# Kernel optimization log

Hardware: AMD Instinct MI355X
Metric: run time of the kernel (lower is better)

Reference implementation:

```python
import jax, jax.numpy as jnp
import numpy as np


def setup_inputs() -> dict:
    key = jax.random.key(0)
    kq, kk, kv = jax.random.split(key, 3)
    B, H, S, D = 2, 16, 2048, 128
    Q = jax.random.normal(kq, (B, H, S, D), dtype=jnp.float32)
    K = jax.random.normal(kk, (B, H, S, D), dtype=jnp.float32)
    V = jax.random.normal(kv, (B, H, S, D), dtype=jnp.float32)
    return {"Q": Q, "K": K, "V": V}


def reference(Q, K, V):
    # Unscaled, unmasked attention: softmax(Q K^T) V
    score = jnp.einsum('bhqd,bhkd->bhqk', Q, K)  # [B,H,S,S]
    attn = jax.nn.softmax(score, axis=-1)
    context = jnp.einsum('bhqk,bhkd->bhqd', attn, V)  # [B,H,S,D]
    return context
```

## Files before the change

kernel.cpp:

```cpp
#include <hip/hip_runtime.h>
#include <stdint.h>

#define BH_N 32
#define S_N  2048
#define D_N  128
#define BK   64
#define NT   (S_N / BK)
#define QW   32
#define BQ   128

#define LOG2E 1.4426950408889634f

typedef __bf16    bf16x8 __attribute__((ext_vector_type(8)));
typedef _Float16  f16x8  __attribute__((ext_vector_type(8)));
typedef float     f32x4  __attribute__((ext_vector_type(4)));

union FragU { uint4 u4; uint32_t u[4]; bf16x8 b; };
union FragH { uint4 u4; uint32_t u[4]; f16x8 h; _Float16 e[8]; };

__device__ __forceinline__ uint32_t pack_bf16(float lo, float hi) {
  uint32_t ul = __float_as_uint(lo) + 0x8000u;
  uint32_t uh = __float_as_uint(hi) + 0x8000u;
  return __builtin_amdgcn_perm(uh, ul, 0x07060302u);
}

__device__ __forceinline__ void gl_lds16(const uint16_t* g, uint16_t* l) {
  __builtin_amdgcn_global_load_lds(
      (const __attribute__((address_space(1))) uint32_t*)g,
      (__attribute__((address_space(3))) uint32_t*)l, 16, 0, 0);
}

__global__ __launch_bounds__(256) void prep_kernel(const float* __restrict__ Kg,
                                                   uint16_t* __restrict__ Ko,
                                                   const float* __restrict__ Vg,
                                                   uint16_t* __restrict__ Vtg) {
  if (blockIdx.x < 4096) {
    const int idx = blockIdx.x * 256 + threadIdx.x;
    const int rg = idx >> 4;
    const int g = idx & 15;
    const float* src = Kg + (size_t)idx * 8;
    float4 a = *(const float4*)(src);
    float4 b = *(const float4*)(src + 4);
    FragH w;
    w.e[0] = (_Float16)a.x; w.e[1] = (_Float16)a.y;
    w.e[2] = (_Float16)a.z; w.e[3] = (_Float16)a.w;
    w.e[4] = (_Float16)b.x; w.e[5] = (_Float16)b.y;
    w.e[6] = (_Float16)b.z; w.e[7] = (_Float16)b.w;
    *(uint4*)(Ko + (size_t)rg * 128 + ((g ^ (rg & 7)) * 8)) = w.u4;
    return;
  }
  __shared__ float stg[64][65];
  const int bid = blockIdx.x - 4096;
  const int dt = bid & 1;
  const int st = (bid >> 1) & 31;
  const int bh = bid >> 6;
  const int tid = threadIdx.x;
  {
    const int r = tid >> 4;
    const int c = (tid & 15) * 4;
    const float* Vb = Vg + ((size_t)bh * S_N + (size_t)st * 64) * D_N + dt * 64;
#pragma unroll
    for (int i = 0; i < 4; ++i) {
      float4 x = *(const float4*)(Vb + (size_t)(r + i * 16) * D_N + c);
      stg[r + i * 16][c + 0] = x.x;
      stg[r + i * 16][c + 1] = x.y;
      stg[r + i * 16][c + 2] = x.z;
      stg[r + i * 16][c + 3] = x.w;
    }
  }
  __syncthreads();
  uint16_t* Vo = Vtg + ((size_t)(bh * 32 + st) * 128 + dt * 64) * 64;
  const int gp = tid & 7;
  const int k0 = (gp & 4) * 8 + (gp & 3) * 4;
#pragma unroll
  for (int it = 0; it < 2; ++it) {
    const int drl = it * 32 + (tid >> 3);
    const int d = dt * 64 + drl;
    uint4 w;
    w.x = pack_bf16(stg[k0 + 0][drl], stg[k0 + 1][drl]);
    w.y = pack_bf16(stg[k0 + 2][drl], stg[k0 + 3][drl]);
    w.z = pack_bf16(stg[k0 + 16][drl], stg[k0 + 17][drl]);
    w.w = pack_bf16(stg[k0 + 18][drl], stg[k0 + 19][drl]);
    *(uint4*)(Vo + (size_t)drl * 64 + ((gp ^ (d & 7)) * 8)) = w;
  }
}

__global__ __launch_bounds__(256, 2)
void attn_kernel(const float* __restrict__ Qg, const uint16_t* __restrict__ Kimg,
                 const uint16_t* __restrict__ Vimg, float* __restrict__ Og) {
  __shared__ uint16_t k_lds[2][BK * 128];
  __shared__ uint16_t vt_lds[2][D_N * 64];

  const int tid = threadIdx.x;
  const int bid = blockIdx.x;
  const int bh = bid & 31;
  const int qb = bid >> 5;
  const int wave = tid >> 6;
  const int lane = tid & 63;
  const int l15 = lane & 15;
  const int quad = lane >> 4;
  const int sw = l15 & 7;

  const float*    Qb = Qg + (size_t)bh * S_N * D_N;
  float*          Ob = Og + (size_t)bh * S_N * D_N;
  const uint16_t* Kt0 = Kimg + (size_t)bh * 32 * 64 * 128;
  const uint16_t* Vt0 = Vimg + (size_t)bh * 32 * 128 * 64;

  const int q0 = qb * BQ + wave * QW;
  const int phase = ((qb << 1) | (bh & 1)) & 31;

  FragH qh[2][4];
#pragma unroll
  for (int g = 0; g < 2; ++g) {
    const float* qrow = Qb + (size_t)(q0 + g * 16 + l15) * D_N + quad * 8;
#pragma unroll
    for (int kc = 0; kc < 4; ++kc) {
      float4 x0 = *(const float4*)(qrow + kc * 32);
      float4 x1 = *(const float4*)(qrow + kc * 32 + 4);
      qh[g][kc].e[0] = (_Float16)(x0.x * LOG2E);
      qh[g][kc].e[1] = (_Float16)(x0.y * LOG2E);
      qh[g][kc].e[2] = (_Float16)(x0.z * LOG2E);
      qh[g][kc].e[3] = (_Float16)(x0.w * LOG2E);
      qh[g][kc].e[4] = (_Float16)(x1.x * LOG2E);
      qh[g][kc].e[5] = (_Float16)(x1.y * LOG2E);
      qh[g][kc].e[6] = (_Float16)(x1.z * LOG2E);
      qh[g][kc].e[7] = (_Float16)(x1.w * LOG2E);
    }
  }

  f32x4 oacc[2][8];
  const f32x4 zf = {0.f, 0.f, 0.f, 0.f};
#pragma unroll
  for (int g = 0; g < 2; ++g)
#pragma unroll
    for (int mt = 0; mt < 8; ++mt) oacc[g][mt] = zf;
  float lsum[2] = {0.f, 0.f};

  const int lel = lane * 8;
  auto stage = [&](int ktp, int buf) {
    const uint16_t* ks = Kt0 + (size_t)ktp * (64 * 128);
    const uint16_t* vs = Vt0 + (size_t)ktp * (128 * 64);
    uint16_t* kl = &k_lds[buf][0];
    uint16_t* vl = &vt_lds[buf][0];
#pragma unroll
    for (int i = 0; i < 4; ++i) {
      const int off = (wave * 16 + i * 4) * 128;
      gl_lds16(ks + off + lel, kl + off + lel);
    }
#pragma unroll
    for (int i = 0; i < 4; ++i) {
      const int off = (wave * 32 + i * 8) * 64;
      gl_lds16(vs + off + lel, vl + off + lel);
    }
  };

  stage(phase, 0);
  asm volatile("s_waitcnt vmcnt(0)" ::: "memory");
  __syncthreads();

#pragma unroll 2
  for (int kt = 0; kt < NT; ++kt) {
    const int cur = kt & 1;
    if (kt + 1 < NT) stage((kt + 1 + phase) & 31, cur ^ 1);

    const uint16_t* kl = &k_lds[cur][0];
    const uint16_t* vl = &vt_lds[cur][0];

    f32x4 sacc[2][4];
    __builtin_amdgcn_s_setprio(1);
#pragma unroll
    for (int kc = 0; kc < 4; ++kc) {
#pragma unroll
      for (int mt = 0; mt < 4; ++mt) {
        FragH a;
        a.u4 = *(const uint4*)(kl + (mt * 16 + l15) * 128 + (((kc * 4 + quad) ^ sw) * 8));
#pragma unroll
        for (int g = 0; g < 2; ++g) {
          f32x4 c = (kc == 0) ? zf : sacc[g][mt];
          sacc[g][mt] = __builtin_amdgcn_mfma_f32_16x16x32_f16(a.h, qh[g][kc].h, c, 0, 0, 0);
        }
      }
    }
    __builtin_amdgcn_s_setprio(0);

#pragma unroll
    for (int half = 0; half < 2; ++half) {
      FragU vf[8];
#pragma unroll
      for (int mt = 0; mt < 8; ++mt)
        vf[mt].u4 = *(const uint4*)(vl + (mt * 16 + l15) * 64 + (((half * 4 + quad) ^ sw) * 8));

      FragU bq[2];
#pragma unroll
      for (int g = 0; g < 2; ++g) {
        const f32x4 s0 = sacc[g][half * 2 + 0];
        const f32x4 s1 = sacc[g][half * 2 + 1];
        float a0 = __builtin_amdgcn_exp2f(s0.x);
        float a1 = __builtin_amdgcn_exp2f(s0.y);
        float a2 = __builtin_amdgcn_exp2f(s0.z);
        float a3 = __builtin_amdgcn_exp2f(s0.w);
        float b0 = __builtin_amdgcn_exp2f(s1.x);
        float b1 = __builtin_amdgcn_exp2f(s1.y);
        float b2 = __builtin_amdgcn_exp2f(s1.z);
        float b3 = __builtin_amdgcn_exp2f(s1.w);
        lsum[g] += ((a0 + a1) + (a2 + a3)) + ((b0 + b1) + (b2 + b3));
        bq[g].u[0] = pack_bf16(a0, a1);
        bq[g].u[1] = pack_bf16(a2, a3);
        bq[g].u[2] = pack_bf16(b0, b1);
        bq[g].u[3] = pack_bf16(b2, b3);
      }
      __builtin_amdgcn_s_setprio(1);
#pragma unroll
      for (int mt = 0; mt < 8; ++mt) {
#pragma unroll
        for (int g = 0; g < 2; ++g) {
          oacc[g][mt] = __builtin_amdgcn_mfma_f32_16x16x32_bf16(vf[mt].b, bq[g].b, oacc[g][mt], 0, 0, 0);
        }
      }
      __builtin_amdgcn_s_setprio(0);
    }

    asm volatile("s_waitcnt vmcnt(0)" ::: "memory");
    __syncthreads();
  }

#pragma unroll
  for (int g = 0; g < 2; ++g) {
    float l = lsum[g];
    l += __shfl_xor(l, 16);
    l += __shfl_xor(l, 32);
    const float rl = 1.0f / l;
#pragma unroll
    for (int mt = 0; mt < 8; ++mt) {
      float4 w;
      w.x = oacc[g][mt].x * rl;
      w.y = oacc[g][mt].y * rl;
      w.z = oacc[g][mt].z * rl;
      w.w = oacc[g][mt].w * rl;
      *(float4*)(Ob + (size_t)(q0 + g * 16 + l15) * D_N + mt * 16 + quad * 4) = w;
    }
  }
}

extern "C" void kernel_launch(void* const* d_in, const int* in_sizes, int n_in,
                              void* d_out, int out_size, void* d_ws, size_t ws_size,
                              hipStream_t stream) {
  const float* Q = (const float*)d_in[0];
  const float* K = (const float*)d_in[1];
  const float* V = (const float*)d_in[2];
  float* O = (float*)d_out;

  const size_t half = (size_t)BH_N * S_N * D_N * sizeof(uint16_t);
  if (ws_size < 2 * half) return;
  uint16_t* Vt = (uint16_t*)d_ws;
  uint16_t* Kh = (uint16_t*)((char*)d_ws + half);

  prep_kernel<<<dim3(4096 + BH_N * 32 * 2), dim3(256), 0, stream>>>(K, Kh, V, Vt);
  attn_kernel<<<dim3(S_N / BQ * BH_N), dim3(256), 0, stream>>>(Q, Kh, Vt, O);
}
```

Before: 195.6 us.

## Software-pipeline QK^T of next tile with softmax and PV of current tile

```diff
diff --git a/kernel.cpp b/kernel.cpp
--- a/kernel.cpp
+++ b/kernel.cpp
@@ -136,17 +136,22 @@
     for (int mt = 0; mt < 8; ++mt) oacc[g][mt] = zf;
   float lsum[2] = {0.f, 0.f};
 
+  f32x4 saccA[2][4];
+  f32x4 saccB[2][4];
+
   const int lel = lane * 8;
-  auto stage = [&](int ktp, int buf) {
+  auto stageK = [&](int ktp, int buf) {
     const uint16_t* ks = Kt0 + (size_t)ktp * (64 * 128);
-    const uint16_t* vs = Vt0 + (size_t)ktp * (128 * 64);
     uint16_t* kl = &k_lds[buf][0];
-    uint16_t* vl = &vt_lds[buf][0];
 #pragma unroll
     for (int i = 0; i < 4; ++i) {
       const int off = (wave * 16 + i * 4) * 128;
       gl_lds16(ks + off + lel, kl + off + lel);
     }
+  };
+  auto stageV = [&](int ktp, int buf) {
+    const uint16_t* vs = Vt0 + (size_t)ktp * (128 * 64);
+    uint16_t* vl = &vt_lds[buf][0];
 #pragma unroll
     for (int i = 0; i < 4; ++i) {
       const int off = (wave * 32 + i * 8) * 64;
@@ -154,19 +159,7 @@
     }
   };
 
-  stage(phase, 0);
-  asm volatile("s_waitcnt vmcnt(0)" ::: "memory");
-  __syncthreads();
-
-#pragma unroll 2
-  for (int kt = 0; kt < NT; ++kt) {
-    const int cur = kt & 1;
-    if (kt + 1 < NT) stage((kt + 1 + phase) & 31, cur ^ 1);
-
-    const uint16_t* kl = &k_lds[cur][0];
-    const uint16_t* vl = &vt_lds[cur][0];
-
-    f32x4 sacc[2][4];
+  auto qk = [&](const uint16_t* kl, f32x4 (&sout_)[2][4]) {
     __builtin_amdgcn_s_setprio(1);
 #pragma unroll
     for (int kc = 0; kc < 4; ++kc) {
@@ -176,25 +169,25 @@
         a.u4 = *(const uint4*)(kl + (mt * 16 + l15) * 128 + (((kc * 4 + quad) ^ sw) * 8));
 #pragma unroll
         for (int g = 0; g < 2; ++g) {
-          f32x4 c = (kc == 0) ? zf : sacc[g][mt];
-          sacc[g][mt] = __builtin_amdgcn_mfma_f32_16x16x32_f16(a.h, qh[g][kc].h, c, 0, 0, 0);
+          f32x4 c = (kc == 0) ? zf : sout_[g][mt];
+          sout_[g][mt] = __builtin_amdgcn_mfma_f32_16x16x32_f16(a.h, qh[g][kc].h, c, 0, 0, 0);
         }
       }
     }
     __builtin_amdgcn_s_setprio(0);
-
+  };
+
+  auto body = [&](int t, f32x4 (&sin_)[2][4], f32x4 (&sout_)[2][4]) {
+    if (t + 2 < NT) stageK((t + 2 + phase) & 31, t & 1);
+    if (t + 1 < NT) stageV((t + 1 + phase) & 31, (t + 1) & 1);
+
+    FragU bq[2][2];
 #pragma unroll
     for (int half = 0; half < 2; ++half) {
-      FragU vf[8];
-#pragma unroll
-      for (int mt = 0; mt < 8; ++mt)
-        vf[mt].u4 = *(const uint4*)(vl + (mt * 16 + l15) * 64 + (((half * 4 + quad) ^ sw) * 8));
-
-      FragU bq[2];
 #pragma unroll
       for (int g = 0; g < 2; ++g) {
-        const f32x4 s0 = sacc[g][half * 2 + 0];
-        const f32x4 s1 = sacc[g][half * 2 + 1];
+        const f32x4 s0 = sin_[g][half * 2 + 0];
+        const f32x4 s1 = sin_[g][half * 2 + 1];
         float a0 = __builtin_amdgcn_exp2f(s0.x);
         float a1 = __builtin_amdgcn_exp2f(s0.y);
         float a2 = __builtin_amdgcn_exp2f(s0.z);
@@ -204,17 +197,28 @@
         float b2 = __builtin_amdgcn_exp2f(s1.z);
         float b3 = __builtin_amdgcn_exp2f(s1.w);
         lsum[g] += ((a0 + a1) + (a2 + a3)) + ((b0 + b1) + (b2 + b3));
-        bq[g].u[0] = pack_bf16(a0, a1);
-        bq[g].u[1] = pack_bf16(a2, a3);
-        bq[g].u[2] = pack_bf16(b0, b1);
-        bq[g].u[3] = pack_bf16(b2, b3);
+        bq[half][g].u[0] = pack_bf16(a0, a1);
+        bq[half][g].u[1] = pack_bf16(a2, a3);
+        bq[half][g].u[2] = pack_bf16(b0, b1);
+        bq[half][g].u[3] = pack_bf16(b2, b3);
       }
+    }
+
+    if (t + 1 < NT) qk(&k_lds[(t + 1) & 1][0], sout_);
+
+    const uint16_t* vl = &vt_lds[t & 1][0];
+#pragma unroll
+    for (int half = 0; half < 2; ++half) {
+      FragU vf[8];
+#pragma unroll
+      for (int mt = 0; mt < 8; ++mt)
+        vf[mt].u4 = *(const uint4*)(vl + (mt * 16 + l15) * 64 + (((half * 4 + quad) ^ sw) * 8));
       __builtin_amdgcn_s_setprio(1);
 #pragma unroll
       for (int mt = 0; mt < 8; ++mt) {
 #pragma unroll
         for (int g = 0; g < 2; ++g) {
-          oacc[g][mt] = __builtin_amdgcn_mfma_f32_16x16x32_bf16(vf[mt].b, bq[g].b, oacc[g][mt], 0, 0, 0);
+          oacc[g][mt] = __builtin_amdgcn_mfma_f32_16x16x32_bf16(vf[mt].b, bq[half][g].b, oacc[g][mt], 0, 0, 0);
         }
       }
       __builtin_amdgcn_s_setprio(0);
@@ -222,6 +226,19 @@
 
     asm volatile("s_waitcnt vmcnt(0)" ::: "memory");
     __syncthreads();
+  };
+
+  stageK(phase, 0);
+  stageV(phase, 0);
+  stageK((1 + phase) & 31, 1);
+  asm volatile("s_waitcnt vmcnt(0)" ::: "memory");
+  __syncthreads();
+  qk(&k_lds[0][0], saccA);
+  __syncthreads();
+
+  for (int t2 = 0; t2 < NT; t2 += 2) {
+    body(t2 + 0, saccA, saccB);
+    body(t2 + 1, saccB, saccA);
   }
 
 #pragma unroll
```

Result: slower. 211.5 us (+8.1%).

## Load V fragments directly from global memory into registers, bypassing LDS

Applied to the files above, without the earlier changes.

```diff
diff --git a/kernel.cpp b/kernel.cpp
--- a/kernel.cpp
+++ b/kernel.cpp
@@ -89,7 +89,6 @@
 void attn_kernel(const float* __restrict__ Qg, const uint16_t* __restrict__ Kimg,
                  const uint16_t* __restrict__ Vimg, float* __restrict__ Og) {
   __shared__ uint16_t k_lds[2][BK * 128];
-  __shared__ uint16_t vt_lds[2][D_N * 64];
 
   const int tid = threadIdx.x;
   const int bid = blockIdx.x;
@@ -137,34 +136,34 @@
   float lsum[2] = {0.f, 0.f};
 
   const int lel = lane * 8;
-  auto stage = [&](int ktp, int buf) {
+  auto stageK = [&](int ktp, int buf) {
     const uint16_t* ks = Kt0 + (size_t)ktp * (64 * 128);
-    const uint16_t* vs = Vt0 + (size_t)ktp * (128 * 64);
     uint16_t* kl = &k_lds[buf][0];
-    uint16_t* vl = &vt_lds[buf][0];
 #pragma unroll
     for (int i = 0; i < 4; ++i) {
       const int off = (wave * 16 + i * 4) * 128;
       gl_lds16(ks + off + lel, kl + off + lel);
     }
-#pragma unroll
-    for (int i = 0; i < 4; ++i) {
-      const int off = (wave * 32 + i * 8) * 64;
-      gl_lds16(vs + off + lel, vl + off + lel);
-    }
   };
 
-  stage(phase, 0);
+  stageK(phase, 0);
   asm volatile("s_waitcnt vmcnt(0)" ::: "memory");
   __syncthreads();
 
 #pragma unroll 2
   for (int kt = 0; kt < NT; ++kt) {
     const int cur = kt & 1;
-    if (kt + 1 < NT) stage((kt + 1 + phase) & 31, cur ^ 1);
+    if (kt + 1 < NT) stageK((kt + 1 + phase) & 31, cur ^ 1);
+
+    const uint16_t* vg = Vt0 + (size_t)((kt + phase) & 31) * (128 * 64);
+    FragU vf0[8], vf1[8];
+#pragma unroll
+    for (int mt = 0; mt < 8; ++mt) {
+      vf0[mt].u4 = *(const uint4*)(vg + (mt * 16 + l15) * 64 + (((0 * 4 + quad) ^ sw) * 8));
+      vf1[mt].u4 = *(const uint4*)(vg + (mt * 16 + l15) * 64 + (((1 * 4 + quad) ^ sw) * 8));
+    }
 
     const uint16_t* kl = &k_lds[cur][0];
-    const uint16_t* vl = &vt_lds[cur][0];
 
     f32x4 sacc[2][4];
     __builtin_amdgcn_s_setprio(1);
@@ -183,18 +182,12 @@
     }
     __builtin_amdgcn_s_setprio(0);
 
-#pragma unroll
-    for (int half = 0; half < 2; ++half) {
-      FragU vf[8];
-#pragma unroll
-      for (int mt = 0; mt < 8; ++mt)
-        vf[mt].u4 = *(const uint4*)(vl + (mt * 16 + l15) * 64 + (((half * 4 + quad) ^ sw) * 8));
-
+    {
       FragU bq[2];
 #pragma unroll
       for (int g = 0; g < 2; ++g) {
-        const f32x4 s0 = sacc[g][half * 2 + 0];
-        const f32x4 s1 = sacc[g][half * 2 + 1];
+        const f32x4 s0 = sacc[g][0];
+        const f32x4 s1 = sacc[g][1];
         float a0 = __builtin_amdgcn_exp2f(s0.x);
         float a1 = __builtin_amdgcn_exp2f(s0.y);
         float a2 = __builtin_amdgcn_exp2f(s0.z);
@@ -214,7 +207,37 @@
       for (int mt = 0; mt < 8; ++mt) {
 #pragma unroll
         for (int g = 0; g < 2; ++g) {
-          oacc[g][mt] = __builtin_amdgcn_mfma_f32_16x16x32_bf16(vf[mt].b, bq[g].b, oacc[g][mt], 0, 0, 0);
+          oacc[g][mt] = __builtin_amdgcn_mfma_f32_16x16x32_bf16(vf0[mt].b, bq[g].b, oacc[g][mt], 0, 0, 0);
+        }
+      }
+      __builtin_amdgcn_s_setprio(0);
+    }
+    {
+      FragU bq[2];
+#pragma unroll
+      for (int g = 0; g < 2; ++g) {
+        const f32x4 s0 = sacc[g][2];
+        const f32x4 s1 = sacc[g][3];
+        float a0 = __builtin_amdgcn_exp2f(s0.x);
+        float a1 = __builtin_amdgcn_exp2f(s0.y);
+        float a2 = __builtin_amdgcn_exp2f(s0.z);
+        float a3 = __builtin_amdgcn_exp2f(s0.w);
+        float b0 = __builtin_amdgcn_exp2f(s1.x);
+        float b1 = __builtin_amdgcn_exp2f(s1.y);
+        float b2 = __builtin_amdgcn_exp2f(s1.z);
+        float b3 = __builtin_amdgcn_exp2f(s1.w);
+        lsum[g] += ((a0 + a1) + (a2 + a3)) + ((b0 + b1) + (b2 + b3));
+        bq[g].u[0] = pack_bf16(a0, a1);
+        bq[g].u[1] = pack_bf16(a2, a3);
+        bq[g].u[2] = pack_bf16(b0, b1);
+        bq[g].u[3] = pack_bf16(b2, b3);
+      }
+      __builtin_amdgcn_s_setprio(1);
+#pragma unroll
+      for (int mt = 0; mt < 8; ++mt) {
+#pragma unroll
+        for (int g = 0; g < 2; ++g) {
+          oacc[g][mt] = __builtin_amdgcn_mfma_f32_16x16x32_bf16(vf1[mt].b, bq[g].b, oacc[g][mt], 0, 0, 0);
         }
       }
       __builtin_amdgcn_s_setprio(0);
```

New measurement: 209.9 us. 1.07x slower.

## Use 8 waves of 16 query rows each instead of 4 waves of 32

Applied to the files above, without the earlier changes.

```diff
diff --git a/kernel.cpp b/kernel.cpp
--- a/kernel.cpp
+++ b/kernel.cpp
@@ -6,7 +6,7 @@
 #define D_N  128
 #define BK   64
 #define NT   (S_N / BK)
-#define QW   32
+#define QW   16
 #define BQ   128
 
 #define LOG2E 1.4426950408889634f
@@ -85,7 +85,7 @@
   }
 }
 
-__global__ __launch_bounds__(256, 2)
+__global__ __launch_bounds__(512, 4)
 void attn_kernel(const float* __restrict__ Qg, const uint16_t* __restrict__ Kimg,
                  const uint16_t* __restrict__ Vimg, float* __restrict__ Og) {
   __shared__ uint16_t k_lds[2][BK * 128];
@@ -109,32 +109,29 @@
   const int q0 = qb * BQ + wave * QW;
   const int phase = ((qb << 1) | (bh & 1)) & 31;
 
-  FragH qh[2][4];
-#pragma unroll
-  for (int g = 0; g < 2; ++g) {
-    const float* qrow = Qb + (size_t)(q0 + g * 16 + l15) * D_N + quad * 8;
+  FragH qh[4];
+  {
+    const float* qrow = Qb + (size_t)(q0 + l15) * D_N + quad * 8;
 #pragma unroll
     for (int kc = 0; kc < 4; ++kc) {
       float4 x0 = *(const float4*)(qrow + kc * 32);
       float4 x1 = *(const float4*)(qrow + kc * 32 + 4);
-      qh[g][kc].e[0] = (_Float16)(x0.x * LOG2E);
-      qh[g][kc].e[1] = (_Float16)(x0.y * LOG2E);
-      qh[g][kc].e[2] = (_Float16)(x0.z * LOG2E);
-      qh[g][kc].e[3] = (_Float16)(x0.w * LOG2E);
-      qh[g][kc].e[4] = (_Float16)(x1.x * LOG2E);
-      qh[g][kc].e[5] = (_Float16)(x1.y * LOG2E);
-      qh[g][kc].e[6] = (_Float16)(x1.z * LOG2E);
-      qh[g][kc].e[7] = (_Float16)(x1.w * LOG2E);
-    }
-  }
-
-  f32x4 oacc[2][8];
+      qh[kc].e[0] = (_Float16)(x0.x * LOG2E);
+      qh[kc].e[1] = (_Float16)(x0.y * LOG2E);
+      qh[kc].e[2] = (_Float16)(x0.z * LOG2E);
+      qh[kc].e[3] = (_Float16)(x0.w * LOG2E);
+      qh[kc].e[4] = (_Float16)(x1.x * LOG2E);
+      qh[kc].e[5] = (_Float16)(x1.y * LOG2E);
+      qh[kc].e[6] = (_Float16)(x1.z * LOG2E);
+      qh[kc].e[7] = (_Float16)(x1.w * LOG2E);
+    }
+  }
+
+  f32x4 oacc[8];
   const f32x4 zf = {0.f, 0.f, 0.f, 0.f};
 #pragma unroll
-  for (int g = 0; g < 2; ++g)
-#pragma unroll
-    for (int mt = 0; mt < 8; ++mt) oacc[g][mt] = zf;
-  float lsum[2] = {0.f, 0.f};
+  for (int mt = 0; mt < 8; ++mt) oacc[mt] = zf;
+  float lsum = 0.f;
 
   const int lel = lane * 8;
   auto stage = [&](int ktp, int buf) {
@@ -143,13 +140,13 @@
     uint16_t* kl = &k_lds[buf][0];
     uint16_t* vl = &vt_lds[buf][0];
 #pragma unroll
-    for (int i = 0; i < 4; ++i) {
-      const int off = (wave * 16 + i * 4) * 128;
+    for (int i = 0; i < 2; ++i) {
+      const int off = (wave * 8 + i * 4) * 128;
       gl_lds16(ks + off + lel, kl + off + lel);
     }
 #pragma unroll
-    for (int i = 0; i < 4; ++i) {
-      const int off = (wave * 32 + i * 8) * 64;
+    for (int i = 0; i < 2; ++i) {
+      const int off = (wave * 16 + i * 8) * 64;
       gl_lds16(vs + off + lel, vl + off + lel);
     }
   };
@@ -166,7 +163,7 @@
     const uint16_t* kl = &k_lds[cur][0];
     const uint16_t* vl = &vt_lds[cur][0];
 
-    f32x4 sacc[2][4];
+    f32x4 sacc[4];
     __builtin_amdgcn_s_setprio(1);
 #pragma unroll
     for (int kc = 0; kc < 4; ++kc) {
@@ -174,11 +171,8 @@
       for (int mt = 0; mt < 4; ++mt) {
         FragH a;
         a.u4 = *(const uint4*)(kl + (mt * 16 + l15) * 128 + (((kc * 4 + quad) ^ sw) * 8));
-#pragma unroll
-        for (int g = 0; g < 2; ++g) {
-          f32x4 c = (kc == 0) ? zf : sacc[g][mt];
-          sacc[g][mt] = __builtin_amdgcn_mfma_f32_16x16x32_f16(a.h, qh[g][kc].h, c, 0, 0, 0);
-        }
+        f32x4 c = (kc == 0) ? zf : sacc[mt];
+        sacc[mt] = __builtin_amdgcn_mfma_f32_16x16x32_f16(a.h, qh[kc].h, c, 0, 0, 0);
       }
     }
     __builtin_amdgcn_s_setprio(0);
@@ -190,11 +184,10 @@
       for (int mt = 0; mt < 8; ++mt)
         vf[mt].u4 = *(const uint4*)(vl + (mt * 16 + l15) * 64 + (((half * 4 + quad) ^ sw) * 8));
 
-      FragU bq[2];
-#pragma unroll
-      for (int g = 0; g < 2; ++g) {
-        const f32x4 s0 = sacc[g][half * 2 + 0];
-        const f32x4 s1 = sacc[g][half * 2 + 1];
+      FragU bq;
+      {
+        const f32x4 s0 = sacc[half * 2 + 0];
+        const f32x4 s1 = sacc[half * 2 + 1];
         float a0 = __builtin_amdgcn_exp2f(s0.x);
         float a1 = __builtin_amdgcn_exp2f(s0.y);
         float a2 = __builtin_amdgcn_exp2f(s0.z);
@@ -203,19 +196,16 @@
         float b1 = __builtin_amdgcn_exp2f(s1.y);
         float b2 = __builtin_amdgcn_exp2f(s1.z);
         float b3 = __builtin_amdgcn_exp2f(s1.w);
-        lsum[g] += ((a0 + a1) + (a2 + a3)) + ((b0 + b1) + (b2 + b3));
-        bq[g].u[0] = pack_bf16(a0, a1);
-        bq[g].u[1] = pack_bf16(a2, a3);
-        bq[g].u[2] = pack_bf16(b0, b1);
-        bq[g].u[3] = pack_bf16(b2, b3);
+        lsum += ((a0 + a1) + (a2 + a3)) + ((b0 + b1) + (b2 + b3));
+        bq.u[0] = pack_bf16(a0, a1);
+        bq.u[1] = pack_bf16(a2, a3);
+        bq.u[2] = pack_bf16(b0, b1);
+        bq.u[3] = pack_bf16(b2, b3);
       }
       __builtin_amdgcn_s_setprio(1);
 #pragma unroll
       for (int mt = 0; mt < 8; ++mt) {
-#pragma unroll
-        for (int g = 0; g < 2; ++g) {
-          oacc[g][mt] = __builtin_amdgcn_mfma_f32_16x16x32_bf16(vf[mt].b, bq[g].b, oacc[g][mt], 0, 0, 0);
-        }
+        oacc[mt] = __builtin_amdgcn_mfma_f32_16x16x32_bf16(vf[mt].b, bq.b, oacc[mt], 0, 0, 0);
       }
       __builtin_amdgcn_s_setprio(0);
     }
@@ -224,20 +214,19 @@
     __syncthreads();
   }
 
-#pragma unroll
-  for (int g = 0; g < 2; ++g) {
-    float l = lsum[g];
+  {
+    float l = lsum;
     l += __shfl_xor(l, 16);
     l += __shfl_xor(l, 32);
     const float rl = 1.0f / l;
 #pragma unroll
     for (int mt = 0; mt < 8; ++mt) {
       float4 w;
-      w.x = oacc[g][mt].x * rl;
-      w.y = oacc[g][mt].y * rl;
-      w.z = oacc[g][mt].z * rl;
-      w.w = oacc[g][mt].w * rl;
-      *(float4*)(Ob + (size_t)(q0 + g * 16 + l15) * D_N + mt * 16 + quad * 4) = w;
+      w.x = oacc[mt].x * rl;
+      w.y = oacc[mt].y * rl;
+      w.z = oacc[mt].z * rl;
+      w.w = oacc[mt].w * rl;
+      *(float4*)(Ob + (size_t)(q0 + l15) * D_N + mt * 16 + quad * 4) = w;
     }
   }
 }
@@ -256,5 +245,5 @@
   uint16_t* Kh = (uint16_t*)((char*)d_ws + half);
 
   prep_kernel<<<dim3(4096 + BH_N * 32 * 2), dim3(256), 0, stream>>>(K, Kh, V, Vt);
-  attn_kernel<<<dim3(S_N / BQ * BH_N), dim3(256), 0, stream>>>(Q, Kh, Vt, O);
-}
+  attn_kernel<<<dim3(S_N / BQ * BH_N), dim3(512), 0, stream>>>(Q, Kh, Vt, O);
+}
```

Measured after the change: 248.0 us. 26.8% more time.
